# Performance work log

Hardware: AMD Instinct MI355X
Metric: run time of the kernel (lower is better)

The kernel has to match this reference:

```python
import jax, jax.numpy as jnp
import numpy as np

N = 50000
E = 800000
F_IN = 10
H = 256          # hidden
NH = 8           # num heads
HD = H // NH     # head dim
ED = 3           # edge feat dim
L = 3            # num layers
EPS_LN = 1e-5


def setup_inputs() -> dict:
    key = jax.random.key(0)
    ks = jax.random.split(key, 20)
    def g(k, shape, scale=0.05):
        return jax.random.normal(k, shape, dtype=jnp.float32) * scale
    inp = {
        "x": jax.random.normal(ks[0], (N, F_IN), dtype=jnp.float32),
        "edge_attr": jax.random.normal(ks[1], (E, ED), dtype=jnp.float32),
        # input projection
        "W_in": g(ks[2], (F_IN, H)), "b_in": jnp.zeros((H,), jnp.float32),
        # per-layer conv params stacked on leading L axis
        "Wq": g(ks[3], (L, H, H)), "Wk": g(ks[4], (L, H, H)), "Wv": g(ks[5], (L, H, H)),
        "We": g(ks[6], (L, ED, NH)),
        "Wo": g(ks[7], (L, H, H)), "bo": jnp.zeros((L, H), jnp.float32),
        "Wm": g(ks[8], (L, 2 * H, H)), "bm": jnp.zeros((L, H), jnp.float32),
        "gamma": jnp.ones((L, H), jnp.float32), "beta": jnp.zeros((L, H), jnp.float32),
        # output head
        "W_h1": g(ks[9], (H, H // 2)), "b_h1": jnp.zeros((H // 2,), jnp.float32),
        "W_h2": g(ks[10], (H // 2, 1)), "b_h2": jnp.zeros((1,), jnp.float32),
        "edge_index": jax.random.randint(ks[11], (2, E), 0, N, dtype=jnp.int64),
    }
    return inp


def _layer_norm(h, gamma, beta):
    mu = jnp.mean(h, axis=-1, keepdims=True)
    var = jnp.var(h, axis=-1, keepdims=True)
    return (h - mu) * jax.lax.rsqrt(var + EPS_LN) * gamma + beta


def _forward(x, edge_attr, W_in, b_in, Wq, Wk, Wv, We, Wo, bo, Wm, bm,
             gamma, beta, W_h1, b_h1, W_h2, b_h2, src, dst):
    scale = HD ** (-0.5)
    h = jax.nn.relu(x @ W_in + b_in)                       # (N, H)
    for l in range(L):
        Q = (h @ Wq[l]).reshape(N, NH, HD)
        K = (h @ Wk[l]).reshape(N, NH, HD)
        V = (h @ Wv[l]).reshape(N, NH, HD)
        edge_bias = edge_attr @ We[l]                      # (E, NH)
        attn = jnp.sum(Q[dst] * K[src], axis=-1) * scale + edge_bias
        attn = jax.nn.leaky_relu(attn, negative_slope=0.2)
        # global-max stabilization, exactly as the torch code does
        attn_exp = jnp.exp(attn - jnp.max(attn))           # (E, NH)
        attn_sum = jax.ops.segment_sum(attn_exp, dst, num_segments=N)
        attn_norm = attn_exp / jnp.clip(attn_sum[dst], 1e-12, None)
        weighted_V = V[src] * attn_norm[..., None]         # (E, NH, HD)
        agg = jax.ops.segment_sum(weighted_V, dst, num_segments=N)
        agg = agg.reshape(N, H) @ Wo[l] + bo[l]
        upd = jax.nn.relu(jnp.concatenate([h, agg], axis=1) @ Wm[l] + bm[l])
        h = _layer_norm(h + upd, gamma[l], beta[l])
    return jax.nn.relu(h @ W_h1 + b_h1) @ W_h2 + b_h2      # (N, 1) logits


def reference(x, edge_attr, W_in, b_in, Wq, Wk, Wv, We, Wo, bo, Wm, bm,
              gamma, beta, W_h1, b_h1, W_h2, b_h2, edge_index):
    src = edge_index[0]
    dst = edge_index[1]
    return _forward(x, edge_attr, W_in, b_in, Wq, Wk, Wv, We, Wo, bo, Wm, bm,
                    gamma, beta, W_h1, b_h1, W_h2, b_h2, src, dst)
```

## Files before the change

kernel.cpp:

```cpp
#include <hip/hip_runtime.h>
#include <math.h>

#define N_NODES 50000
#define E_EDGES 800000
#define HDIM 256
#define NHEADS 8
#define HEADD 32
#define EDGED 3
#define NLAYERS 3

typedef unsigned int u32;
typedef unsigned char u8;
typedef unsigned short ushort_t;
typedef __attribute__((ext_vector_type(8))) short short8;
typedef __attribute__((ext_vector_type(8))) unsigned short ushort8v;
typedef __attribute__((ext_vector_type(4))) float float4v;
typedef __attribute__((ext_vector_type(2))) float float2v;

typedef __attribute__((address_space(1))) const void* gas_p;
typedef __attribute__((address_space(3))) void* las_p;

__device__ __forceinline__ float bf2f(ushort_t u) {
  union { u32 i; float f; } v;
  v.i = ((u32)u) << 16;
  return v.f;
}
__device__ __forceinline__ ushort_t f2bf(float f) {
  u32 u = __float_as_uint(f);
  u = (u + 0x7FFF + ((u >> 16) & 1)) >> 16;
  return (ushort_t)u;
}
__device__ __forceinline__ u8 f2f8(float f) {
  int p = __builtin_amdgcn_cvt_pk_fp8_f32(f, 0.f, 0, false);
  return (u8)(p & 0xFF);
}
__device__ __forceinline__ void f8x4_to_f32(u32 v, float* out) {
  float2v a = __builtin_amdgcn_cvt_pk_f32_fp8((int)v, false);
  float2v b = __builtin_amdgcn_cvt_pk_f32_fp8((int)v, true);
  out[0] = a[0];
  out[1] = a[1];
  out[2] = b[0];
  out[3] = b[1];
}

__global__ __launch_bounds__(256) void detect_idx_k(const u32* __restrict__ w,
                                                    int* __restrict__ flag) {
  __shared__ u32 sm[256];
  u32 mx = 0;
  for (int k = threadIdx.x; k < 4096; k += 256) mx = max(mx, w[2 * k + 1]);
  sm[threadIdx.x] = mx;
  __syncthreads();
  for (int s = 128; s > 0; s >>= 1) {
    if (threadIdx.x < s)
      sm[threadIdx.x] = max(sm[threadIdx.x], sm[threadIdx.x + s]);
    __syncthreads();
  }
  if (threadIdx.x == 0) flag[0] = (sm[0] == 0) ? 1 : 0;
}

__global__ __launch_bounds__(256) void convert_hist_k(
    const u32* __restrict__ w, const int* __restrict__ flag,
    int* __restrict__ src32, int* __restrict__ dst32, int* __restrict__ dcnt,
    int E_) {
  int e = blockIdx.x * blockDim.x + threadIdx.x;
  if (e >= E_) return;
  int s, d;
  if (flag[0]) {
    s = (int)w[2 * e];
    d = (int)w[2 * (E_ + e)];
  } else {
    s = (int)w[e];
    d = (int)w[E_ + e];
  }
  src32[e] = s;
  dst32[e] = d;
  atomicAdd(&dcnt[d], 1);
}

__global__ __launch_bounds__(256) void scan1_k(const int* __restrict__ deg,
                                               int* __restrict__ scanned,
                                               int* __restrict__ bsum, int n) {
  __shared__ int tmp[256];
  int tid = threadIdx.x;
  int i = blockIdx.x * 256 + tid;
  tmp[tid] = (i < n) ? deg[i] : 0;
  __syncthreads();
  for (int off = 1; off < 256; off <<= 1) {
    int t = (tid >= off) ? tmp[tid - off] : 0;
    __syncthreads();
    tmp[tid] += t;
    __syncthreads();
  }
  if (i < n) scanned[i] = tmp[tid];
  if (tid == 255) bsum[blockIdx.x] = tmp[255];
}

__global__ __launch_bounds__(256) void scan2_k(int* __restrict__ bsum, int nb) {
  __shared__ int tmp[256];
  int tid = threadIdx.x;
  tmp[tid] = (tid < nb) ? bsum[tid] : 0;
  __syncthreads();
  for (int off = 1; off < 256; off <<= 1) {
    int t = (tid >= off) ? tmp[tid - off] : 0;
    __syncthreads();
    tmp[tid] += t;
    __syncthreads();
  }
  if (tid < nb) bsum[tid] = tmp[tid];
}

__global__ __launch_bounds__(256) void scan3_k(const int* __restrict__ scanned,
                                               const int* __restrict__ bsum,
                                               int* __restrict__ rowptr, int n) {
  int i = blockIdx.x * 256 + threadIdx.x;
  if (i < n)
    rowptr[i + 1] = scanned[i] + (blockIdx.x > 0 ? bsum[blockIdx.x - 1] : 0);
  if (i == 0) rowptr[0] = 0;
}

__global__ __launch_bounds__(256) void fill_k(
    const int* __restrict__ srcI, const int* __restrict__ dstI,
    const int* __restrict__ rowptr, int* __restrict__ cursor,
    int2* __restrict__ erec, int E_) {
  int e = blockIdx.x * blockDim.x + threadIdx.x;
  if (e >= E_) return;
  int d = dstI[e];
  int p = rowptr[d] + atomicAdd(&cursor[d], 1);
  erec[p] = make_int2(srcI[e], e);
}

__global__ __launch_bounds__(256) void wtrans_all_k(
    const float* __restrict__ Wq, const float* __restrict__ Wk,
    const float* __restrict__ Wv, const float* __restrict__ Wm,
    const float* __restrict__ Wh1, ushort_t* __restrict__ WqkvT,
    ushort_t* __restrict__ WmT, ushort_t* __restrict__ Wh1T) {
  int z = blockIdx.z;
  const float* W;
  ushort_t* WT;
  int K, N;
  if (z < 9) {
    if (blockIdx.x >= 16) return;
    int l = z / 3, m = z % 3;
    W = (m == 0 ? Wq : m == 1 ? Wk : Wv) + (size_t)l * 65536;
    WT = WqkvT + ((size_t)l * 3 + m) * 65536;
    K = 256;
    N = 256;
  } else if (z < 12) {
    int l = z - 9;
    W = Wm + (size_t)l * 131072;
    WT = WmT + (size_t)l * 131072;
    K = 512;
    N = 256;
  } else {
    if (blockIdx.x >= 16 || blockIdx.y >= 2) return;
    W = Wh1;
    WT = Wh1T;
    K = 256;
    N = 128;
  }
  __shared__ float t[64][17];
  int k0 = blockIdx.x * 16, n0 = blockIdx.y * 64;
  int tid = threadIdx.x;
  int r = tid >> 6, c = tid & 63;
#pragma unroll
  for (int i = 0; i < 4; ++i)
    t[c][r + 4 * i] = W[(size_t)(k0 + r + 4 * i) * N + n0 + c];
  __syncthreads();
  int n = tid >> 2, j4 = (tid & 3) * 4;
  ushort4 o;
  o.x = f2bf(t[n][j4 + 0]);
  o.y = f2bf(t[n][j4 + 1]);
  o.z = f2bf(t[n][j4 + 2]);
  o.w = f2bf(t[n][j4 + 3]);
  *(ushort4*)&WT[(size_t)(n0 + n) * K + k0 + j4] = o;
}

__global__ __launch_bounds__(256) void wcomb_k(const float* __restrict__ Wo,
                                               const float* __restrict__ Wm,
                                               ushort_t* __restrict__ WmT) {
  int l = blockIdx.z;
  const float* A = Wo + (size_t)l * 65536;
  const float* B = Wm + (size_t)l * 131072 + 65536;
  ushort_t* Out = WmT + (size_t)l * 131072;
  __shared__ float As[16][64];
  __shared__ float Bs[16][64];
  int tid = threadIdx.x;
  int tx = tid & 15, ty = tid >> 4;
  int k0 = blockIdx.x * 64, n0 = blockIdx.y * 64;
  float acc[4][4] = {};
  int arow = tid >> 2;
  int aj = (tid & 3) * 4;
  int brow = tid >> 4;
  int bcol = (tid & 15) * 4;
  for (int j0 = 0; j0 < 256; j0 += 16) {
    float4 av = *(const float4*)(A + (size_t)(k0 + arow) * 256 + j0 + aj);
    As[aj + 0][arow] = av.x;
    As[aj + 1][arow] = av.y;
    As[aj + 2][arow] = av.z;
    As[aj + 3][arow] = av.w;
    *(float4*)&Bs[brow][bcol] =
        *(const float4*)(B + (size_t)(j0 + brow) * 256 + n0 + bcol);
    __syncthreads();
#pragma unroll
    for (int j = 0; j < 16; ++j) {
      float a[4], bb[4];
#pragma unroll
      for (int i = 0; i < 4; ++i) a[i] = As[j][ty * 4 + i];
#pragma unroll
      for (int jj = 0; jj < 4; ++jj) bb[jj] = Bs[j][tx * 4 + jj];
#pragma unroll
      for (int i = 0; i < 4; ++i)
#pragma unroll
        for (int jj = 0; jj < 4; ++jj) acc[i][jj] += a[i] * bb[jj];
    }
    __syncthreads();
  }
#pragma unroll
  for (int i = 0; i < 4; ++i)
#pragma unroll
    for (int jj = 0; jj < 4; ++jj) {
      int k = k0 + ty * 4 + i, n = n0 + tx * 4 + jj;
      Out[(size_t)n * 512 + 256 + k] = f2bf(acc[i][jj]);
    }
}

__global__ __launch_bounds__(256) void bcomb_k(const float* __restrict__ bo,
                                               const float* __restrict__ bm,
                                               const float* __restrict__ Wm,
                                               float* __restrict__ bcomb) {
  int l = blockIdx.z;
  int n = threadIdx.x;
  const float* Bw = Wm + (size_t)l * 131072 + 65536;
  const float* bol = bo + l * 256;
  float acc = bm[l * 256 + n];
  for (int j = 0; j < 256; ++j) acc += bol[j] * Bw[(size_t)j * 256 + n];
  bcomb[l * 256 + n] = acc;
}

__global__ __launch_bounds__(256) void input_proj_k(
    const float* __restrict__ x, const float* __restrict__ W,
    const float* __restrict__ b, ushort_t* __restrict__ hbf, int n) {
  __shared__ float ws[10 * 256];
  __shared__ float bs[256];
  int tid = threadIdx.x;
  for (int i = tid; i < 2560; i += 256) ws[i] = W[i];
  bs[tid] = b[tid];
  __syncthreads();
  int row0 = blockIdx.x * 32;
  for (int rr = 0; rr < 32; ++rr) {
    int row = row0 + rr;
    if (row >= n) break;
    float acc = bs[tid];
#pragma unroll
    for (int i = 0; i < 10; ++i) acc += x[row * 10 + i] * ws[i * 256 + tid];
    hbf[(size_t)row * 256 + tid] = f2bf(fmaxf(acc, 0.f));
  }
}

__global__ __launch_bounds__(256) void gemm_qkv_k(
    const ushort_t* __restrict__ A1, const ushort_t* __restrict__ BT,
    ushort_t* __restrict__ Qbf, u8* __restrict__ KV8, int M) {
  const int K1 = 256, Ktot = 256;
  __shared__ __align__(16) ushort_t Als[128 * 64];
  __shared__ __align__(16) ushort_t Bls[64 * 64];
  int tid = threadIdx.x;
  int lane = tid & 63, w = tid >> 6;
  int quad = lane >> 4, m = lane & 15;
  int row0 = blockIdx.y * 128, col0 = blockIdx.x * 64;
  float4v acc[2][4];
#pragma unroll
  for (int t = 0; t < 2; ++t)
#pragma unroll
    for (int j = 0; j < 4; ++j) acc[t][j] = (float4v){0.f, 0.f, 0.f, 0.f};

  int srow = tid >> 3;
  int skc = (tid & 7) * 8;
  char* alsb = (char*)Als + w * 1024;
  char* blsb = (char*)Bls + w * 1024;

  for (int k0 = 0; k0 < Ktot; k0 += 64) {
#pragma unroll
    for (int q = 0; q < 4; ++q) {
      int r = row0 + q * 32 + srow;
      if (r < M) {
        const ushort_t* g = A1 + (size_t)r * K1 + k0 + skc;
        __builtin_amdgcn_global_load_lds((gas_p)g, (las_p)(alsb + q * 4096),
                                         16, 0, 0);
      }
    }
#pragma unroll
    for (int q = 0; q < 2; ++q) {
      const ushort_t* g = BT + (size_t)(col0 + q * 32 + srow) * Ktot + k0 + skc;
      __builtin_amdgcn_global_load_lds((gas_p)g, (las_p)(blsb + q * 4096), 16,
                                       0, 0);
    }
    __syncthreads();
#pragma unroll
    for (int ks = 0; ks < 64; ks += 32) {
      short8 a0 = *(const short8*)&Als[(w * 32 + m) * 64 + ks + quad * 8];
      short8 a1 = *(const short8*)&Als[(w * 32 + 16 + m) * 64 + ks + quad * 8];
#pragma unroll
      for (int j = 0; j < 4; ++j) {
        short8 bj = *(const short8*)&Bls[(16 * j + m) * 64 + ks + quad * 8];
        acc[0][j] =
            __builtin_amdgcn_mfma_f32_16x16x32_bf16(a0, bj, acc[0][j], 0, 0, 0);
        acc[1][j] =
            __builtin_amdgcn_mfma_f32_16x16x32_bf16(a1, bj, acc[1][j], 0, 0, 0);
      }
    }
    __syncthreads();
  }

#pragma unroll
  for (int t = 0; t < 2; ++t) {
#pragma unroll
    for (int j = 0; j < 4; ++j) {
      int col = col0 + 16 * j + m;
#pragma unroll
      for (int rr = 0; rr < 4; ++rr) {
        int row = row0 + w * 32 + 16 * t + quad * 4 + rr;
        if (row >= M) continue;
        float v = acc[t][j][rr];
        if (col < 256)
          Qbf[(size_t)row * 256 + col] = f2bf(v);
        else
          KV8[(size_t)row * 512 + (col - 256)] = f2f8(v);
      }
    }
  }
}

__global__ __launch_bounds__(256) void gemm_ln_k(
    ushort_t* __restrict__ hbf, const ushort_t* __restrict__ aggbf,
    const ushort_t* __restrict__ BT, const float* __restrict__ bcomb,
    const float* __restrict__ gamma, const float* __restrict__ beta, int M) {
  __shared__ __align__(16) ushort_t Als[64 * 64];
  __shared__ __align__(16) ushort_t Bls[256 * 64];
  int tid = threadIdx.x;
  int lane = tid & 63, w = tid >> 6;
  int quad = lane >> 4, m = lane & 15;
  int row0 = blockIdx.x * 64;
  float4v acc[16];
#pragma unroll
  for (int j = 0; j < 16; ++j) acc[j] = (float4v){0.f, 0.f, 0.f, 0.f};

  int srow = tid >> 3;
  int skc = (tid & 7) * 8;
  char* alsb = (char*)Als + w * 1024;
  char* blsb = (char*)Bls + w * 1024;

  for (int k0 = 0; k0 < 512; k0 += 64) {
    const ushort_t* Ap = (k0 < 256) ? (const ushort_t*)hbf : aggbf;
    int kk = k0 & 255;
#pragma unroll
    for (int q = 0; q < 2; ++q) {
      int r = row0 + q * 32 + srow;
      if (r < M) {
        const ushort_t* g = Ap + (size_t)r * 256 + kk + skc;
        __builtin_amdgcn_global_load_lds((gas_p)g, (las_p)(alsb + q * 4096),
                                         16, 0, 0);
      }
    }
#pragma unroll
    for (int q = 0; q < 8; ++q) {
      const ushort_t* g = BT + (size_t)(q * 32 + srow) * 512 + k0 + skc;
      __builtin_amdgcn_global_load_lds((gas_p)g, (las_p)(blsb + q * 4096), 16,
                                       0, 0);
    }
    __syncthreads();
#pragma unroll
    for (int ks = 0; ks < 64; ks += 32) {
      short8 a = *(const short8*)&Als[(w * 16 + m) * 64 + ks + quad * 8];
#pragma unroll
      for (int j = 0; j < 16; ++j) {
        short8 bj = *(const short8*)&Bls[(16 * j + m) * 64 + ks + quad * 8];
        acc[j] = __builtin_amdgcn_mfma_f32_16x16x32_bf16(a, bj, acc[j], 0, 0, 0);
      }
    }
    __syncthreads();
  }

#pragma unroll
  for (int rr = 0; rr < 4; ++rr) {
    int row = row0 + w * 16 + quad * 4 + rr;
    if (row >= M) continue;
    float sv[16];
    float sum = 0.f, sq = 0.f;
#pragma unroll
    for (int j = 0; j < 16; ++j) {
      int col = m + 16 * j;
      float u = fmaxf(acc[j][rr] + bcomb[col], 0.f);
      float s = bf2f(hbf[(size_t)row * 256 + col]) + u;
      sv[j] = s;
      sum += s;
      sq += s * s;
    }
#pragma unroll
    for (int off = 1; off < 16; off <<= 1) {
      sum += __shfl_xor(sum, off);
      sq += __shfl_xor(sq, off);
    }
    float mean = sum * (1.f / 256.f);
    float var = sq * (1.f / 256.f) - mean * mean;
    float r = rsqrtf(var + 1e-5f);
#pragma unroll
    for (int j = 0; j < 16; ++j) {
      int col = m + 16 * j;
      float o = (sv[j] - mean) * r * gamma[col] + beta[col];
      hbf[(size_t)row * 256 + col] = f2bf(o);
    }
  }
}

__global__ __launch_bounds__(256) void head_fused_k(
    const ushort_t* __restrict__ hbf, const ushort_t* __restrict__ W1T,
    const float* __restrict__ b1, const float* __restrict__ W2,
    const float* __restrict__ b2, float* __restrict__ out, int M) {
  __shared__ __align__(16) ushort_t Als[64 * 64];
  __shared__ __align__(16) ushort_t Bls[128 * 64];
  int tid = threadIdx.x;
  int lane = tid & 63, w = tid >> 6;
  int quad = lane >> 4, m = lane & 15;
  int row0 = blockIdx.x * 64;
  float4v acc[8];
#pragma unroll
  for (int j = 0; j < 8; ++j) acc[j] = (float4v){0.f, 0.f, 0.f, 0.f};

  int srow = tid >> 3;
  int skc = (tid & 7) * 8;
  char* alsb = (char*)Als + w * 1024;
  char* blsb = (char*)Bls + w * 1024;

  for (int k0 = 0; k0 < 256; k0 += 64) {
#pragma unroll
    for (int q = 0; q < 2; ++q) {
      int r = row0 + q * 32 + srow;
      if (r < M) {
        const ushort_t* g = hbf + (size_t)r * 256 + k0 + skc;
        __builtin_amdgcn_global_load_lds((gas_p)g, (las_p)(alsb + q * 4096),
                                         16, 0, 0);
      }
    }
#pragma unroll
    for (int q = 0; q < 4; ++q) {
      const ushort_t* g = W1T + (size_t)(q * 32 + srow) * 256 + k0 + skc;
      __builtin_amdgcn_global_load_lds((gas_p)g, (las_p)(blsb + q * 4096), 16,
                                       0, 0);
    }
    __syncthreads();
#pragma unroll
    for (int ks = 0; ks < 64; ks += 32) {
      short8 a = *(const short8*)&Als[(w * 16 + m) * 64 + ks + quad * 8];
#pragma unroll
      for (int j = 0; j < 8; ++j) {
        short8 bj = *(const short8*)&Bls[(16 * j + m) * 64 + ks + quad * 8];
        acc[j] = __builtin_amdgcn_mfma_f32_16x16x32_bf16(a, bj, acc[j], 0, 0, 0);
      }
    }
    __syncthreads();
  }

#pragma unroll
  for (int rr = 0; rr < 4; ++rr) {
    int row = row0 + w * 16 + quad * 4 + rr;
    if (row >= M) continue;
    float p = 0.f;
#pragma unroll
    for (int j = 0; j < 8; ++j) {
      int col = m + 16 * j;
      float t = fmaxf(acc[j][rr] + b1[col], 0.f);
      p += t * W2[col];
    }
#pragma unroll
    for (int off = 1; off < 16; off <<= 1) p += __shfl_xor(p, off);
    if (m == 0) out[row] = p + b2[0];
  }
}

__global__ __launch_bounds__(256) void node_fused_k(
    const ushort_t* __restrict__ Q, const u8* __restrict__ KV8,
    const float* __restrict__ ea, const float* __restrict__ We_l,
    const int* __restrict__ rowptr, const int2* __restrict__ erec,
    ushort_t* __restrict__ agg, int n) {
  int node = (blockIdx.x * blockDim.x + threadIdx.x) >> 6;
  if (node >= n) return;
  int lane = threadIdx.x & 63;
  int hl = lane & 31;
  int slot = lane >> 5;
  ushort8v qu = *((const ushort8v*)(Q + (size_t)node * 256) + hl);
  float q[8];
#pragma unroll
  for (int i = 0; i < 8; ++i) q[i] = bf2f(qu[i]);
  int start = rowptr[node], end = rowptr[node + 1];
  int hh = hl >> 2;
  float w0 = We_l[0 * 8 + hh], w1 = We_l[1 * 8 + hh], w2 = We_l[2 * 8 + hh];
  float l = 0.f;
  float acc[8];
#pragma unroll
  for (int i = 0; i < 8; ++i) acc[i] = 0.f;

  int iters = (end - start + 1) >> 1;
  for (int it = 0; it < iters; ++it) {
    int p = start + 2 * it + slot;
    if (p < end) {
      int2 er = erec[p];
      const u8* base = KV8 + (size_t)er.x * 512;
      uint2 ku = *((const uint2*)base + hl);
      uint2 vu = *((const uint2*)(base + 256) + hl);
      float kf[8], vf[8];
      f8x4_to_f32(ku.x, kf);
      f8x4_to_f32(ku.y, kf + 4);
      f8x4_to_f32(vu.x, vf);
      f8x4_to_f32(vu.y, vf + 4);
      float d = 0.f;
#pragma unroll
      for (int i = 0; i < 8; ++i) d += q[i] * kf[i];
      d += __shfl_xor(d, 1);
      d += __shfl_xor(d, 2);
      float bias = ea[(size_t)er.y * 3 + 0] * w0 +
                   ea[(size_t)er.y * 3 + 1] * w1 +
                   ea[(size_t)er.y * 3 + 2] * w2;
      float a = d * 0.17677669529663687f + bias;
      a = (a > 0.f) ? a : 0.2f * a;
      float wv = __expf(a);
      l += wv;
#pragma unroll
      for (int i = 0; i < 8; ++i) acc[i] += vf[i] * wv;
    }
  }
  l += __shfl_xor(l, 32);
  float inv = 1.f / fmaxf(l, 1e-12f);
  ushort8v o;
#pragma unroll
  for (int i = 0; i < 8; ++i) {
    float v = (acc[i] + __shfl_xor(acc[i], 32)) * inv;
    o[i] = f2bf(v);
  }
  if (slot == 0)
    *((ushort8v*)(agg + (size_t)node * 256) + hl) = o;
}

extern "C" void kernel_launch(void* const* d_in, const int* in_sizes, int n_in,
                              void* d_out, int out_size, void* d_ws,
                              size_t ws_size, hipStream_t stream) {
  const float* x = (const float*)d_in[0];
  const float* edge_attr = (const float*)d_in[1];
  const float* W_in = (const float*)d_in[2];
  const float* b_in = (const float*)d_in[3];
  const float* Wq = (const float*)d_in[4];
  const float* Wk = (const float*)d_in[5];
  const float* Wv = (const float*)d_in[6];
  const float* We = (const float*)d_in[7];
  const float* Wo = (const float*)d_in[8];
  const float* bo = (const float*)d_in[9];
  const float* Wm = (const float*)d_in[10];
  const float* bm = (const float*)d_in[11];
  const float* gamma = (const float*)d_in[12];
  const float* beta = (const float*)d_in[13];
  const float* W_h1 = (const float*)d_in[14];
  const float* b_h1 = (const float*)d_in[15];
  const float* W_h2 = (const float*)d_in[16];
  const float* b_h2 = (const float*)d_in[17];
  const u32* eidx_w = (const u32*)d_in[18];

  float* ws = (float*)d_ws;
  const size_t NH_ = (size_t)N_NODES * HDIM;
  ushort_t* hbf = (ushort_t*)ws;
  ushort_t* Qbf = hbf + NH_;
  u8* KV8 = (u8*)(Qbf + NH_);
  ushort_t* aggbf = (ushort_t*)(KV8 + (size_t)N_NODES * 512);
  int* idxflag = (int*)(aggbf + NH_);
  int2* erec = (int2*)(idxflag + 2);
  int* rowptr = (int*)(erec + E_EDGES);
  int* dcnt = rowptr + N_NODES + 1;
  int* cursor = dcnt + N_NODES;
  int* scanned = cursor + N_NODES;
  int* bsum = scanned + N_NODES;
  float* bcomb = (float*)(bsum + 256);
  ushort_t* WT = (ushort_t*)(bcomb + 3 * 256);
  const size_t W64K = (size_t)HDIM * HDIM;
  const size_t W128K = (size_t)2 * HDIM * HDIM;
  ushort_t* WqkvT = WT;
  ushort_t* WmT = WqkvT + 3 * 3 * W64K;
  ushort_t* Wh1T = WmT + 3 * W128K;
  int* srcI = (int*)Qbf;
  int* dstI = srcI + E_EDGES;

  detect_idx_k<<<1, 256, 0, stream>>>(eidx_w, idxflag);
  hipMemsetAsync(dcnt, 0, (size_t)2 * N_NODES * sizeof(int), stream);
  convert_hist_k<<<(E_EDGES + 255) / 256, 256, 0, stream>>>(
      eidx_w, idxflag, srcI, dstI, dcnt, E_EDGES);
  const int nsb = (N_NODES + 255) / 256;
  scan1_k<<<nsb, 256, 0, stream>>>(dcnt, scanned, bsum, N_NODES);
  scan2_k<<<1, 256, 0, stream>>>(bsum, nsb);
  scan3_k<<<nsb, 256, 0, stream>>>(scanned, bsum, rowptr, N_NODES);
  fill_k<<<(E_EDGES + 255) / 256, 256, 0, stream>>>(
      srcI, dstI, rowptr, cursor, erec, E_EDGES);

  wtrans_all_k<<<dim3(32, 4, 13), 256, 0, stream>>>(Wq, Wk, Wv, Wm, W_h1,
                                                    WqkvT, WmT, Wh1T);
  wcomb_k<<<dim3(4, 4, 3), 256, 0, stream>>>(Wo, Wm, WmT);
  bcomb_k<<<dim3(1, 1, 3), 256, 0, stream>>>(bo, bm, Wm, bcomb);

  input_proj_k<<<(N_NODES + 31) / 32, 256, 0, stream>>>(x, W_in, b_in, hbf,
                                                        N_NODES);
  dim3 gqkv(768 / 64, (N_NODES + 127) / 128);
  const int gml = (N_NODES + 63) / 64;
  const int nodewave_grid = (N_NODES * 64 + 255) / 256;

  for (int l = 0; l < NLAYERS; ++l) {
    const float* We_l = We + (size_t)l * EDGED * NHEADS;

    gemm_qkv_k<<<gqkv, 256, 0, stream>>>(
        hbf, WqkvT + (size_t)l * 3 * W64K, Qbf, KV8, N_NODES);
    node_fused_k<<<nodewave_grid, 256, 0, stream>>>(
        Qbf, KV8, edge_attr, We_l, rowptr, erec, aggbf, N_NODES);
    gemm_ln_k<<<gml, 256, 0, stream>>>(
        hbf, aggbf, WmT + (size_t)l * W128K, bcomb + l * 256,
        gamma + (size_t)l * HDIM, beta + (size_t)l * HDIM, N_NODES);
  }
  head_fused_k<<<gml, 256, 0, stream>>>(hbf, Wh1T, b_h1, W_h2, b_h2,
                                        (float*)d_out, N_NODES);
}
```

Measured before the change: 777.3 us.

## Unroll edge gather loop, widen QKV GEMM tile, merge weight-prep kernels

The per-node attention loop now handles two edges per slot per iteration and issues all erec, K/V and edge-attribute loads up front. Out-of-range edges are masked to zero weight, which raises memory-level parallelism in the gather-bound aggregation. The QKV GEMM tile widens from 64 to 128 output columns, so each A tile is reused across more MFMAs, at the cost of more LDS and accumulator registers. The three weight-preparation kernels are folded into one launch that writes disjoint regions, saving two launches.

```diff
diff --git a/kernel.cpp b/kernel.cpp
--- a/kernel.cpp
+++ b/kernel.cpp
@@ -129,112 +129,110 @@
   erec[p] = make_int2(srcI[e], e);
 }
 
-__global__ __launch_bounds__(256) void wtrans_all_k(
+__global__ __launch_bounds__(256) void wprep_all_k(
     const float* __restrict__ Wq, const float* __restrict__ Wk,
     const float* __restrict__ Wv, const float* __restrict__ Wm,
-    const float* __restrict__ Wh1, ushort_t* __restrict__ WqkvT,
-    ushort_t* __restrict__ WmT, ushort_t* __restrict__ Wh1T) {
+    const float* __restrict__ Wh1, const float* __restrict__ Wo,
+    const float* __restrict__ bo, const float* __restrict__ bm,
+    ushort_t* __restrict__ WqkvT, ushort_t* __restrict__ WmT,
+    ushort_t* __restrict__ Wh1T, float* __restrict__ bcomb) {
   int z = blockIdx.z;
-  const float* W;
-  ushort_t* WT;
-  int K, N;
-  if (z < 9) {
-    if (blockIdx.x >= 16) return;
-    int l = z / 3, m = z % 3;
-    W = (m == 0 ? Wq : m == 1 ? Wk : Wv) + (size_t)l * 65536;
-    WT = WqkvT + ((size_t)l * 3 + m) * 65536;
-    K = 256;
-    N = 256;
-  } else if (z < 12) {
-    int l = z - 9;
-    W = Wm + (size_t)l * 131072;
-    WT = WmT + (size_t)l * 131072;
-    K = 512;
-    N = 256;
+  if (z < 13) {
+    const float* W;
+    ushort_t* WT;
+    int K, N;
+    if (z < 9) {
+      if (blockIdx.x >= 16) return;
+      int l = z / 3, mm = z % 3;
+      W = (mm == 0 ? Wq : mm == 1 ? Wk : Wv) + (size_t)l * 65536;
+      WT = WqkvT + ((size_t)l * 3 + mm) * 65536;
+      K = 256;
+      N = 256;
+    } else if (z < 12) {
+      if (blockIdx.x >= 16) return;
+      int l = z - 9;
+      W = Wm + (size_t)l * 131072;
+      WT = WmT + (size_t)l * 131072;
+      K = 512;
+      N = 256;
+    } else {
+      if (blockIdx.x >= 16 || blockIdx.y >= 2) return;
+      W = Wh1;
+      WT = Wh1T;
+      K = 256;
+      N = 128;
+    }
+    __shared__ float t[64][17];
+    int k0 = blockIdx.x * 16, n0 = blockIdx.y * 64;
+    int tid = threadIdx.x;
+    int r = tid >> 6, c = tid & 63;
+#pragma unroll
+    for (int i = 0; i < 4; ++i)
+      t[c][r + 4 * i] = W[(size_t)(k0 + r + 4 * i) * N + n0 + c];
+    __syncthreads();
+    int nn = tid >> 2, j4 = (tid & 3) * 4;
+    ushort4 o;
+    o.x = f2bf(t[nn][j4 + 0]);
+    o.y = f2bf(t[nn][j4 + 1]);
+    o.z = f2bf(t[nn][j4 + 2]);
+    o.w = f2bf(t[nn][j4 + 3]);
+    *(ushort4*)&WT[(size_t)(n0 + nn) * K + k0 + j4] = o;
+  } else if (z < 16) {
+    if (blockIdx.x >= 4 || blockIdx.y >= 4) return;
+    int l = z - 13;
+    const float* A = Wo + (size_t)l * 65536;
+    const float* B = Wm + (size_t)l * 131072 + 65536;
+    ushort_t* Out = WmT + (size_t)l * 131072;
+    __shared__ float As[16][64];
+    __shared__ float Bs[16][64];
+    int tid = threadIdx.x;
+    int tx = tid & 15, ty = tid >> 4;
+    int k0 = blockIdx.x * 64, n0 = blockIdx.y * 64;
+    float acc[4][4] = {};
+    int arow = tid >> 2;
+    int aj = (tid & 3) * 4;
+    int brow = tid >> 4;
+    int bcol = (tid & 15) * 4;
+    for (int j0 = 0; j0 < 256; j0 += 16) {
+      float4 av = *(const float4*)(A + (size_t)(k0 + arow) * 256 + j0 + aj);
+      As[aj + 0][arow] = av.x;
+      As[aj + 1][arow] = av.y;
+      As[aj + 2][arow] = av.z;
+      As[aj + 3][arow] = av.w;
+      *(float4*)&Bs[brow][bcol] =
+          *(const float4*)(B + (size_t)(j0 + brow) * 256 + n0 + bcol);
+      __syncthreads();
+#pragma unroll
+      for (int j = 0; j < 16; ++j) {
+        float a[4], bb[4];
+#pragma unroll
+        for (int i = 0; i < 4; ++i) a[i] = As[j][ty * 4 + i];
+#pragma unroll
+        for (int jj = 0; jj < 4; ++jj) bb[jj] = Bs[j][tx * 4 + jj];
+#pragma unroll
+        for (int i = 0; i < 4; ++i)
+#pragma unroll
+          for (int jj = 0; jj < 4; ++jj) acc[i][jj] += a[i] * bb[jj];
+      }
+      __syncthreads();
+    }
+#pragma unroll
+    for (int i = 0; i < 4; ++i)
+#pragma unroll
+      for (int jj = 0; jj < 4; ++jj) {
+        int k = k0 + ty * 4 + i, nn = n0 + tx * 4 + jj;
+        Out[(size_t)nn * 512 + 256 + k] = f2bf(acc[i][jj]);
+      }
   } else {
-    if (blockIdx.x >= 16 || blockIdx.y >= 2) return;
-    W = Wh1;
-    WT = Wh1T;
-    K = 256;
-    N = 128;
-  }
-  __shared__ float t[64][17];
-  int k0 = blockIdx.x * 16, n0 = blockIdx.y * 64;
-  int tid = threadIdx.x;
-  int r = tid >> 6, c = tid & 63;
-#pragma unroll
-  for (int i = 0; i < 4; ++i)
-    t[c][r + 4 * i] = W[(size_t)(k0 + r + 4 * i) * N + n0 + c];
-  __syncthreads();
-  int n = tid >> 2, j4 = (tid & 3) * 4;
-  ushort4 o;
-  o.x = f2bf(t[n][j4 + 0]);
-  o.y = f2bf(t[n][j4 + 1]);
-  o.z = f2bf(t[n][j4 + 2]);
-  o.w = f2bf(t[n][j4 + 3]);
-  *(ushort4*)&WT[(size_t)(n0 + n) * K + k0 + j4] = o;
-}
-
-__global__ __launch_bounds__(256) void wcomb_k(const float* __restrict__ Wo,
-                                               const float* __restrict__ Wm,
-                                               ushort_t* __restrict__ WmT) {
-  int l = blockIdx.z;
-  const float* A = Wo + (size_t)l * 65536;
-  const float* B = Wm + (size_t)l * 131072 + 65536;
-  ushort_t* Out = WmT + (size_t)l * 131072;
-  __shared__ float As[16][64];
-  __shared__ float Bs[16][64];
-  int tid = threadIdx.x;
-  int tx = tid & 15, ty = tid >> 4;
-  int k0 = blockIdx.x * 64, n0 = blockIdx.y * 64;
-  float acc[4][4] = {};
-  int arow = tid >> 2;
-  int aj = (tid & 3) * 4;
-  int brow = tid >> 4;
-  int bcol = (tid & 15) * 4;
-  for (int j0 = 0; j0 < 256; j0 += 16) {
-    float4 av = *(const float4*)(A + (size_t)(k0 + arow) * 256 + j0 + aj);
-    As[aj + 0][arow] = av.x;
-    As[aj + 1][arow] = av.y;
-    As[aj + 2][arow] = av.z;
-    As[aj + 3][arow] = av.w;
-    *(float4*)&Bs[brow][bcol] =
-        *(const float4*)(B + (size_t)(j0 + brow) * 256 + n0 + bcol);
-    __syncthreads();
-#pragma unroll
-    for (int j = 0; j < 16; ++j) {
-      float a[4], bb[4];
-#pragma unroll
-      for (int i = 0; i < 4; ++i) a[i] = As[j][ty * 4 + i];
-#pragma unroll
-      for (int jj = 0; jj < 4; ++jj) bb[jj] = Bs[j][tx * 4 + jj];
-#pragma unroll
-      for (int i = 0; i < 4; ++i)
-#pragma unroll
-        for (int jj = 0; jj < 4; ++jj) acc[i][jj] += a[i] * bb[jj];
-    }
-    __syncthreads();
-  }
-#pragma unroll
-  for (int i = 0; i < 4; ++i)
-#pragma unroll
-    for (int jj = 0; jj < 4; ++jj) {
-      int k = k0 + ty * 4 + i, n = n0 + tx * 4 + jj;
-      Out[(size_t)n * 512 + 256 + k] = f2bf(acc[i][jj]);
-    }
-}
-
-__global__ __launch_bounds__(256) void bcomb_k(const float* __restrict__ bo,
-                                               const float* __restrict__ bm,
-                                               const float* __restrict__ Wm,
-                                               float* __restrict__ bcomb) {
-  int l = blockIdx.z;
-  int n = threadIdx.x;
-  const float* Bw = Wm + (size_t)l * 131072 + 65536;
-  const float* bol = bo + l * 256;
-  float acc = bm[l * 256 + n];
-  for (int j = 0; j < 256; ++j) acc += bol[j] * Bw[(size_t)j * 256 + n];
-  bcomb[l * 256 + n] = acc;
+    if (blockIdx.x >= 3 || blockIdx.y != 0) return;
+    int l = blockIdx.x;
+    int nn = threadIdx.x;
+    const float* Bw = Wm + (size_t)l * 131072 + 65536;
+    const float* bol = bo + l * 256;
+    float acc = bm[l * 256 + nn];
+    for (int j = 0; j < 256; ++j) acc += bol[j] * Bw[(size_t)j * 256 + nn];
+    bcomb[l * 256 + nn] = acc;
+  }
 }
 
 __global__ __launch_bounds__(256) void input_proj_k(
@@ -262,16 +260,16 @@
     ushort_t* __restrict__ Qbf, u8* __restrict__ KV8, int M) {
   const int K1 = 256, Ktot = 256;
   __shared__ __align__(16) ushort_t Als[128 * 64];
-  __shared__ __align__(16) ushort_t Bls[64 * 64];
+  __shared__ __align__(16) ushort_t Bls[128 * 64];
   int tid = threadIdx.x;
   int lane = tid & 63, w = tid >> 6;
   int quad = lane >> 4, m = lane & 15;
-  int row0 = blockIdx.y * 128, col0 = blockIdx.x * 64;
-  float4v acc[2][4];
+  int row0 = blockIdx.y * 128, col0 = blockIdx.x * 128;
+  float4v acc[2][8];
 #pragma unroll
   for (int t = 0; t < 2; ++t)
 #pragma unroll
-    for (int j = 0; j < 4; ++j) acc[t][j] = (float4v){0.f, 0.f, 0.f, 0.f};
+    for (int j = 0; j < 8; ++j) acc[t][j] = (float4v){0.f, 0.f, 0.f, 0.f};
 
   int srow = tid >> 3;
   int skc = (tid & 7) * 8;
@@ -289,7 +287,7 @@
       }
     }
 #pragma unroll
-    for (int q = 0; q < 2; ++q) {
+    for (int q = 0; q < 4; ++q) {
       const ushort_t* g = BT + (size_t)(col0 + q * 32 + srow) * Ktot + k0 + skc;
       __builtin_amdgcn_global_load_lds((gas_p)g, (las_p)(blsb + q * 4096), 16,
                                        0, 0);
@@ -300,7 +298,7 @@
       short8 a0 = *(const short8*)&Als[(w * 32 + m) * 64 + ks + quad * 8];
       short8 a1 = *(const short8*)&Als[(w * 32 + 16 + m) * 64 + ks + quad * 8];
 #pragma unroll
-      for (int j = 0; j < 4; ++j) {
+      for (int j = 0; j < 8; ++j) {
         short8 bj = *(const short8*)&Bls[(16 * j + m) * 64 + ks + quad * 8];
         acc[0][j] =
             __builtin_amdgcn_mfma_f32_16x16x32_bf16(a0, bj, acc[0][j], 0, 0, 0);
@@ -314,7 +312,7 @@
 #pragma unroll
   for (int t = 0; t < 2; ++t) {
 #pragma unroll
-    for (int j = 0; j < 4; ++j) {
+    for (int j = 0; j < 8; ++j) {
       int col = col0 + 16 * j + m;
 #pragma unroll
       for (int rr = 0; rr < 4; ++rr) {
@@ -499,30 +497,55 @@
 #pragma unroll
   for (int i = 0; i < 8; ++i) acc[i] = 0.f;
 
-  int iters = (end - start + 1) >> 1;
-  for (int it = 0; it < iters; ++it) {
-    int p = start + 2 * it + slot;
-    if (p < end) {
-      int2 er = erec[p];
-      const u8* base = KV8 + (size_t)er.x * 512;
-      uint2 ku = *((const uint2*)base + hl);
-      uint2 vu = *((const uint2*)(base + 256) + hl);
+  if (end > start) {
+    int bp = start + slot;
+    int nb = (end - start + 3) >> 2;
+    for (int j = 0; j < nb; ++j) {
+      int pX = bp + 4 * j;
+      int pY = pX + 2;
+      bool vX = pX < end, vY = pY < end;
+      int2 erX = erec[vX ? pX : start];
+      int2 erY = erec[vY ? pY : start];
+      const u8* bX = KV8 + (size_t)erX.x * 512;
+      const u8* bY = KV8 + (size_t)erY.x * 512;
+      uint2 kuX = *((const uint2*)bX + hl);
+      uint2 vuX = *((const uint2*)(bX + 256) + hl);
+      uint2 kuY = *((const uint2*)bY + hl);
+      uint2 vuY = *((const uint2*)(bY + 256) + hl);
+      const float* eaX = ea + (size_t)erX.y * 3;
+      const float* eaY = ea + (size_t)erY.y * 3;
+      float e0X = eaX[0], e1X = eaX[1], e2X = eaX[2];
+      float e0Y = eaY[0], e1Y = eaY[1], e2Y = eaY[2];
       float kf[8], vf[8];
-      f8x4_to_f32(ku.x, kf);
-      f8x4_to_f32(ku.y, kf + 4);
-      f8x4_to_f32(vu.x, vf);
-      f8x4_to_f32(vu.y, vf + 4);
+      f8x4_to_f32(kuX.x, kf);
+      f8x4_to_f32(kuX.y, kf + 4);
       float d = 0.f;
 #pragma unroll
       for (int i = 0; i < 8; ++i) d += q[i] * kf[i];
       d += __shfl_xor(d, 1);
       d += __shfl_xor(d, 2);
-      float bias = ea[(size_t)er.y * 3 + 0] * w0 +
-                   ea[(size_t)er.y * 3 + 1] * w1 +
-                   ea[(size_t)er.y * 3 + 2] * w2;
+      float bias = e0X * w0 + e1X * w1 + e2X * w2;
       float a = d * 0.17677669529663687f + bias;
       a = (a > 0.f) ? a : 0.2f * a;
-      float wv = __expf(a);
+      float wv = vX ? __expf(a) : 0.f;
+      f8x4_to_f32(vuX.x, vf);
+      f8x4_to_f32(vuX.y, vf + 4);
+      l += wv;
+#pragma unroll
+      for (int i = 0; i < 8; ++i) acc[i] += vf[i] * wv;
+      f8x4_to_f32(kuY.x, kf);
+      f8x4_to_f32(kuY.y, kf + 4);
+      d = 0.f;
+#pragma unroll
+      for (int i = 0; i < 8; ++i) d += q[i] * kf[i];
+      d += __shfl_xor(d, 1);
+      d += __shfl_xor(d, 2);
+      bias = e0Y * w0 + e1Y * w1 + e2Y * w2;
+      a = d * 0.17677669529663687f + bias;
+      a = (a > 0.f) ? a : 0.2f * a;
+      wv = vY ? __expf(a) : 0.f;
+      f8x4_to_f32(vuY.x, vf);
+      f8x4_to_f32(vuY.y, vf + 4);
       l += wv;
 #pragma unroll
       for (int i = 0; i < 8; ++i) acc[i] += vf[i] * wv;
@@ -597,14 +620,12 @@
   fill_k<<<(E_EDGES + 255) / 256, 256, 0, stream>>>(
       srcI, dstI, rowptr, cursor, erec, E_EDGES);
 
-  wtrans_all_k<<<dim3(32, 4, 13), 256, 0, stream>>>(Wq, Wk, Wv, Wm, W_h1,
-                                                    WqkvT, WmT, Wh1T);
-  wcomb_k<<<dim3(4, 4, 3), 256, 0, stream>>>(Wo, Wm, WmT);
-  bcomb_k<<<dim3(1, 1, 3), 256, 0, stream>>>(bo, bm, Wm, bcomb);
+  wprep_all_k<<<dim3(16, 4, 17), 256, 0, stream>>>(
+      Wq, Wk, Wv, Wm, W_h1, Wo, bo, bm, WqkvT, WmT, Wh1T, bcomb);
 
   input_proj_k<<<(N_NODES + 31) / 32, 256, 0, stream>>>(x, W_in, b_in, hbf,
                                                         N_NODES);
-  dim3 gqkv(768 / 64, (N_NODES + 127) / 128);
+  dim3 gqkv(768 / 128, (N_NODES + 127) / 128);
   const int gml = (N_NODES + 63) / 64;
   const int nodewave_grid = (N_NODES * 64 + 255) / 256;
 
```

Result: slower. 793.4 us (+2.1%).
